# Kernel optimization log

Hardware: AMD Instinct MI355X
Metric: run time of the kernel (lower is better)

Reference implementation:

```python
import jax, jax.numpy as jnp
import numpy as np

N_CTRL_U = 64
N_CTRL_V = 64
N_EVAL = 2001  # int(1/0.0005) + 1


def _clamped_knots(p, n_ctrl, dtype):
    """Clamped uniform knot vector on [0,1], length n_ctrl + p + 1."""
    n_internal = n_ctrl - p - 1
    internal = jnp.linspace(0.0, 1.0, n_internal + 2, dtype=dtype)[1:-1]
    return jnp.concatenate([
        jnp.zeros(p + 1, dtype=dtype), internal, jnp.ones(p + 1, dtype=dtype)
    ])


def _find_spans(knots, u, p, n_ctrl):
    """Knot-span index for each parameter (NURBS book A2.1, via searchsorted)."""
    return jnp.clip(jnp.searchsorted(knots, u, side='right') - 1, p, n_ctrl - 1)


def _basis_functions(knots, spans, u, p):
    """Cox-de-Boor nonzero basis functions (NURBS book A2.2), vectorized over u.
    Returns [N, p+1]."""
    Ns = [jnp.ones_like(u)]
    left = {}
    right = {}
    for j in range(1, p + 1):
        left[j] = u - knots[spans + 1 - j]
        right[j] = knots[spans + j] - u
        saved = jnp.zeros_like(u)
        new = []
        for r in range(j):
            temp = Ns[r] / (right[r + 1] + left[j - r])
            new.append(saved + right[r + 1] * temp)
            saved = left[j - r] * temp
        new.append(saved)
        Ns = new
    return jnp.stack(Ns, axis=-1)


def setup_inputs() -> dict:
    key = jax.random.key(0)
    k1, = jax.random.split(key, 1)
    control_points = jax.random.normal(k1, (N_CTRL_U, N_CTRL_V, 3), dtype=jnp.float32)
    params_u = jnp.linspace(0.0, 1.0, N_EVAL, dtype=jnp.float32)
    params_v = jnp.linspace(0.0, 1.0, N_EVAL, dtype=jnp.float32)
    return {"control_points": control_points, "params_u": params_u,
            "params_v": params_v, "degree": 3}


def reference(control_points, params_u, params_v, degree):
    p = int(degree)
    n_u, n_v, d = control_points.shape
    dt = control_points.dtype
    ku = _clamped_knots(p, n_u, dt)
    kv = _clamped_knots(p, n_v, dt)
    su = _find_spans(ku, params_u, p, n_u)          # [Nu]
    sv = _find_spans(kv, params_v, p, n_v)          # [Nv]
    Bu = _basis_functions(ku, su, params_u, p)      # [Nu, p+1]
    Bv = _basis_functions(kv, sv, params_v, p)      # [Nv, p+1]
    off = jnp.arange(p + 1)
    iu = su[:, None] - p + off[None, :]             # [Nu, p+1]
    iv = sv[:, None] - p + off[None, :]             # [Nv, p+1]
    # Contract u first to keep intermediates small: [Nu, p+1, n_v, d] -> [Nu, n_v, d]
    ctrl_u = control_points[iu]                     # gather rows by span
    curve_u = jnp.einsum('ua,uavd->uvd', Bu, ctrl_u)
    # Gather v spans then contract: [Nu, Nv, p+1, d] -> [Nu, Nv, d]
    pts = curve_u[:, iv]
    return jnp.einsum('vb,uvbd->uvd', Bv, pts)
```

## Files before the change

### kernel.cpp

```cpp
#include <hip/hip_runtime.h>

#define N_EVAL 2001
#define NCTRL  64
#define ROWF   6003
#define RPB    4
#define TPB    512
#define GROUPF (RPB * ROWF)

__device__ __forceinline__ float knotv(int i) {
    if (i <= 3) return 0.0f;
    if (i >= NCTRL) return 1.0f;
    return (float)(i - 3) * (1.0f / 61.0f);
}

__device__ __forceinline__ void basis_p3(float u, int& span, float* Ns) {
    int s = 3 + (int)floorf(u * 61.0f);
    s = max(3, min(63, s));
    while (s < 63 && knotv(s + 1) <= u) ++s;
    while (s > 3 && knotv(s) > u) --s;
    float left[4], right[4];
    Ns[0] = 1.0f;
    #pragma unroll
    for (int j = 1; j <= 3; ++j) {
        left[j]  = u - knotv(s + 1 - j);
        right[j] = knotv(s + j) - u;
        float saved = 0.0f;
        #pragma unroll
        for (int r = 0; r < j; ++r) {
            float temp = Ns[r] / (right[r + 1] + left[j - r]);
            Ns[r] = saved + right[r + 1] * temp;
            saved = left[j - r] * temp;
        }
        Ns[j] = saved;
    }
    span = s;
}

__global__ void basis_kernel(const float* __restrict__ pu, const float* __restrict__ pv,
                             float4* __restrict__ Bu4, int* __restrict__ su,
                             float4* __restrict__ bvp) {
    int gid = blockIdx.x * blockDim.x + threadIdx.x;
    if (gid >= N_EVAL) return;
    int s; float N[4];
    basis_p3(pu[gid], s, N);
    Bu4[gid] = make_float4(N[0], N[1], N[2], N[3]);
    su[gid] = s;
    int s2; float M[4];
    basis_p3(pv[gid], s2, M);
    bvp[gid] = make_float4(M[0], M[1], M[2], (float)s2);
}

__device__ __forceinline__ float3 eval_pt(const float4* __restrict__ curve, float4 q) {
    float b3 = 1.0f - q.x - q.y - q.z;
    int iv0 = (int)q.w - 3;
    float4 c0 = curve[iv0 + 0];
    float4 c1 = curve[iv0 + 1];
    float4 c2 = curve[iv0 + 2];
    float4 c3 = curve[iv0 + 3];
    return make_float3(q.x * c0.x + q.y * c1.x + q.z * c2.x + b3 * c3.x,
                       q.x * c0.y + q.y * c1.y + q.z * c2.y + b3 * c3.y,
                       q.x * c0.z + q.y * c1.z + q.z * c2.z + b3 * c3.z);
}

__global__ __launch_bounds__(TPB) void eval_kernel(const float* __restrict__ cp,
                                                   const float4* __restrict__ Bu4,
                                                   const int* __restrict__ su,
                                                   const float4* __restrict__ bvp,
                                                   float* __restrict__ out) {
    __shared__ float4 curve[RPB * NCTRL];

    const int b = blockIdx.x;
    const int t = threadIdx.x;
    const int u0 = b * RPB;
    const int nrows = min(RPB, N_EVAL - u0);

    #pragma unroll
    for (int pass = 0; pass < 2; ++pass) {
        const int w = t + pass * TPB;
        if (w < nrows * (NCTRL * 3)) {
            const int r   = w / (NCTRL * 3);
            const int idx = w - r * (NCTRL * 3);
            const float4 bu = Bu4[u0 + r];
            const int  s_u  = su[u0 + r];
            const int base  = (s_u - 3) * (NCTRL * 3);
            float c = bu.x * cp[base +       idx]
                    + bu.y * cp[base + 192 + idx]
                    + bu.z * cp[base + 384 + idx]
                    + bu.w * cp[base + 576 + idx];
            const int j = idx / 3, d = idx - 3 * j;
            ((float*)curve)[(r * NCTRL + j) * 4 + d] = c;
        }
    }
    __syncthreads();

    const size_t G = (size_t)b * GROUPF;
    float4* outv = (float4*)(out + G);
    const int totalF    = nrows * ROWF;
    const int fullSlots = totalF >> 2;

    #pragma unroll
    for (int k = 0; k < 12; ++k) {
        const int s = k * TPB + t;
        if (s < fullSlots) {
            const int f   = 4 * s;
            const int g1  = f + 3;
            const int r0  = f  / ROWF;
            const int fr0 = f  - r0 * ROWF;
            const int r1  = g1 / ROWF;
            const int fr1 = g1 - r1 * ROWF;
            const int v0  = fr0 / 3;
            const int ph  = fr0 - 3 * v0;
            const int v1  = fr1 / 3;
            const float4 q0 = bvp[v0];
            const float4 q1 = bvp[v1];
            const float3 P0 = eval_pt(curve + r0 * NCTRL, q0);
            const float3 P1 = eval_pt(curve + r1 * NCTRL, q1);
            float4 rr;
            if (ph == 0)      rr = make_float4(P0.x, P0.y, P0.z, P1.x);
            else if (ph == 1) rr = make_float4(P0.y, P0.z, P1.x, P1.y);
            else              rr = make_float4(P0.z, P1.x, P1.y, P1.z);
            outv[s] = rr;
        }
    }

    const int leftover = totalF - 4 * fullSlots;
    if (t < leftover) {
        const int g    = 4 * fullSlots + t;
        const int r    = g / ROWF;
        const int fr   = g - r * ROWF;
        const int v    = fr / 3;
        const int comp = fr - 3 * v;
        const float3 P = eval_pt(curve + r * NCTRL, bvp[v]);
        out[G + g] = (comp == 0) ? P.x : (comp == 1 ? P.y : P.z);
    }
}

extern "C" void kernel_launch(void* const* d_in, const int* in_sizes, int n_in,
                              void* d_out, int out_size, void* d_ws, size_t ws_size,
                              hipStream_t stream) {
    const float* cp = (const float*)d_in[0];
    const float* pu = (const float*)d_in[1];
    const float* pv = (const float*)d_in[2];
    float* out = (float*)d_out;

    float4* Bu4 = (float4*)d_ws;
    float4* bvp = Bu4 + N_EVAL;
    int* su = (int*)(bvp + N_EVAL);

    basis_kernel<<<8, 256, 0, stream>>>(pu, pv, Bu4, su, bvp);

    const int nblocks = (N_EVAL + RPB - 1) / RPB;
    eval_kernel<<<nblocks, TPB, 0, stream>>>(cp, Bu4, su, bvp, out);
}
```

Measured before the change: 84.89 us.

## Fuse basis computation into eval kernel with per-block shared-memory basis tables

Removes the separate basis kernel and workspace round trip. Each block now recomputes all 2001 v-basis entries into shared memory (about 32KB) and its own u-basis rows, and prefetches control points into registers before the sync. Divisions use the hardware reciprocal. In exchange, the v-basis work is repeated in every block and the larger shared-memory footprint may reduce occupancy, though it saves a launch and global reads.

```diff
diff --git a/kernel.cpp b/kernel.cpp
--- a/kernel.cpp
+++ b/kernel.cpp
@@ -13,11 +13,19 @@
     return (float)(i - 3) * (1.0f / 61.0f);
 }
 
-__device__ __forceinline__ void basis_p3(float u, int& span, float* Ns) {
+__device__ __forceinline__ int find_span(float u) {
     int s = 3 + (int)floorf(u * 61.0f);
     s = max(3, min(63, s));
     while (s < 63 && knotv(s + 1) <= u) ++s;
     while (s > 3 && knotv(s) > u) --s;
+    return s;
+}
+
+__device__ __forceinline__ float fdiv_fast(float a, float b) {
+    return a * __builtin_amdgcn_rcpf(b);
+}
+
+__device__ __forceinline__ void basis_from_span(float u, int s, float* Ns) {
     float left[4], right[4];
     Ns[0] = 1.0f;
     #pragma unroll
@@ -27,27 +35,12 @@
         float saved = 0.0f;
         #pragma unroll
         for (int r = 0; r < j; ++r) {
-            float temp = Ns[r] / (right[r + 1] + left[j - r]);
+            float temp = fdiv_fast(Ns[r], right[r + 1] + left[j - r]);
             Ns[r] = saved + right[r + 1] * temp;
             saved = left[j - r] * temp;
         }
         Ns[j] = saved;
     }
-    span = s;
-}
-
-__global__ void basis_kernel(const float* __restrict__ pu, const float* __restrict__ pv,
-                             float4* __restrict__ Bu4, int* __restrict__ su,
-                             float4* __restrict__ bvp) {
-    int gid = blockIdx.x * blockDim.x + threadIdx.x;
-    if (gid >= N_EVAL) return;
-    int s; float N[4];
-    basis_p3(pu[gid], s, N);
-    Bu4[gid] = make_float4(N[0], N[1], N[2], N[3]);
-    su[gid] = s;
-    int s2; float M[4];
-    basis_p3(pv[gid], s2, M);
-    bvp[gid] = make_float4(M[0], M[1], M[2], (float)s2);
 }
 
 __device__ __forceinline__ float3 eval_pt(const float4* __restrict__ curve, float4 q) {
@@ -62,17 +55,61 @@
                        q.x * c0.z + q.y * c1.z + q.z * c2.z + b3 * c3.z);
 }
 
-__global__ __launch_bounds__(TPB) void eval_kernel(const float* __restrict__ cp,
-                                                   const float4* __restrict__ Bu4,
-                                                   const int* __restrict__ su,
-                                                   const float4* __restrict__ bvp,
-                                                   float* __restrict__ out) {
+__global__ __launch_bounds__(TPB, 4) void nurbs_kernel(const float* __restrict__ cp,
+                                                       const float* __restrict__ pu,
+                                                       const float* __restrict__ pv,
+                                                       float* __restrict__ out) {
+    __shared__ float4 bvp[N_EVAL];
     __shared__ float4 curve[RPB * NCTRL];
+    __shared__ float4 bu4s[RPB];
 
     const int b = blockIdx.x;
     const int t = threadIdx.x;
     const int u0 = b * RPB;
     const int nrows = min(RPB, N_EVAL - u0);
+
+    float pvv[4];
+    #pragma unroll
+    for (int k = 0; k < 4; ++k) {
+        int v = t + k * TPB;
+        pvv[k] = pv[min(v, N_EVAL - 1)];
+    }
+
+    float cl[2][4];
+    #pragma unroll
+    for (int pass = 0; pass < 2; ++pass) {
+        const int w = t + pass * TPB;
+        if (w < nrows * (NCTRL * 3)) {
+            const int r   = w / (NCTRL * 3);
+            const int idx = w - r * (NCTRL * 3);
+            const int s_u = find_span(pu[u0 + r]);
+            const int base = (s_u - 3) * (NCTRL * 3);
+            cl[pass][0] = cp[base +       idx];
+            cl[pass][1] = cp[base + 192 + idx];
+            cl[pass][2] = cp[base + 384 + idx];
+            cl[pass][3] = cp[base + 576 + idx];
+        }
+    }
+
+    #pragma unroll
+    for (int k = 0; k < 4; ++k) {
+        const int v = t + k * TPB;
+        if (v < N_EVAL) {
+            const int s2 = find_span(pvv[k]);
+            float M[4];
+            basis_from_span(pvv[k], s2, M);
+            bvp[v] = make_float4(M[0], M[1], M[2], (float)s2);
+        }
+    }
+
+    if (t < nrows) {
+        const float uu = pu[u0 + t];
+        const int s_u = find_span(uu);
+        float Nu[4];
+        basis_from_span(uu, s_u, Nu);
+        bu4s[t] = make_float4(Nu[0], Nu[1], Nu[2], Nu[3]);
+    }
+    __syncthreads();
 
     #pragma unroll
     for (int pass = 0; pass < 2; ++pass) {
@@ -80,13 +117,9 @@
         if (w < nrows * (NCTRL * 3)) {
             const int r   = w / (NCTRL * 3);
             const int idx = w - r * (NCTRL * 3);
-            const float4 bu = Bu4[u0 + r];
-            const int  s_u  = su[u0 + r];
-            const int base  = (s_u - 3) * (NCTRL * 3);
-            float c = bu.x * cp[base +       idx]
-                    + bu.y * cp[base + 192 + idx]
-                    + bu.z * cp[base + 384 + idx]
-                    + bu.w * cp[base + 576 + idx];
+            const float4 bu = bu4s[r];
+            float c = bu.x * cl[pass][0] + bu.y * cl[pass][1]
+                    + bu.z * cl[pass][2] + bu.w * cl[pass][3];
             const int j = idx / 3, d = idx - 3 * j;
             ((float*)curve)[(r * NCTRL + j) * 4 + d] = c;
         }
@@ -142,13 +175,8 @@
     const float* pu = (const float*)d_in[1];
     const float* pv = (const float*)d_in[2];
     float* out = (float*)d_out;
-
-    float4* Bu4 = (float4*)d_ws;
-    float4* bvp = Bu4 + N_EVAL;
-    int* su = (int*)(bvp + N_EVAL);
-
-    basis_kernel<<<8, 256, 0, stream>>>(pu, pv, Bu4, su, bvp);
+    (void)d_ws; (void)ws_size;
 
     const int nblocks = (N_EVAL + RPB - 1) / RPB;
-    eval_kernel<<<nblocks, TPB, 0, stream>>>(cp, Bu4, su, bvp, out);
+    nurbs_kernel<<<nblocks, TPB, 0, stream>>>(cp, pu, pv, out);
 }
```

Measured after the change: 86.61 us. +2.0%, slower.
